# Performance work log

Hardware: AMD Instinct MI355X
Metric: run time of the kernel (lower is better)

## Reference

```python
import jax, jax.numpy as jnp
import numpy as np

N = 100000   # nodes
E = 1600000  # edges (before self-loops)
F_IN = 128
H = 64
G = 512      # graphs in batch


def _add_self_loops(edge_index, n):
    loop = jnp.arange(n, dtype=edge_index.dtype)
    src = jnp.concatenate([edge_index[0], loop])
    dst = jnp.concatenate([edge_index[1], loop])
    return src, dst


def _gcn_norm(src, dst, n):
    # PyG GCNConv: deg over targets with self-loops, norm = d^-1/2[src]*d^-1/2[dst]
    deg = jax.ops.segment_sum(jnp.ones_like(dst, dtype=jnp.float32), dst, num_segments=n)
    dinv = jnp.where(deg > 0, jax.lax.rsqrt(deg), 0.0)
    return dinv[src] * dinv[dst]


def _gcn_conv(x, src, dst, norm, W, b):
    xw = x @ W                                # [N, H]
    msg = xw[src] * norm[:, None]             # [E+N, H] gather + scale
    out = jax.ops.segment_sum(msg, dst, num_segments=x.shape[0])
    return out + b


def setup_inputs() -> dict:
    key = jax.random.key(0)
    ks = jax.random.split(key, 9)
    x = jax.random.normal(ks[0], (N, F_IN), dtype=jnp.float32)
    edge_index = jax.random.randint(ks[1], (2, E), 0, N, dtype=jnp.int32)
    batch = jnp.sort(jax.random.randint(ks[2], (N,), 0, G, dtype=jnp.int32))
    s1 = 1.0 / np.sqrt(F_IN)
    s2 = 1.0 / np.sqrt(H)
    W1 = jax.random.uniform(ks[3], (F_IN, H), jnp.float32, -s1, s1)
    b1 = jnp.zeros((H,), jnp.float32)
    W2 = jax.random.uniform(ks[4], (H, H), jnp.float32, -s2, s2)
    b2 = jnp.zeros((H,), jnp.float32)
    Wl = jax.random.uniform(ks[5], (H, 1), jnp.float32, -s2, s2)
    bl = jnp.zeros((1,), jnp.float32)
    return {"x": x, "edge_index": edge_index, "batch": batch,
            "W1": W1, "b1": b1, "W2": W2, "b2": b2, "Wl": Wl, "bl": bl}


def reference(x, edge_index, batch, W1, b1, W2, b2, Wl, bl):
    n = x.shape[0]
    src, dst = _add_self_loops(edge_index, n)
    norm = _gcn_norm(src, dst, n)
    h = jax.nn.relu(_gcn_conv(x, src, dst, norm, W1, b1))
    h = jax.nn.relu(_gcn_conv(h, src, dst, norm, W2, b2))
    # global mean pool over graphs
    sums = jax.ops.segment_sum(h, batch, num_segments=G)          # [G, H]
    cnt = jax.ops.segment_sum(jnp.ones((n,), jnp.float32), batch, num_segments=G)
    pooled = sums / jnp.maximum(cnt, 1.0)[:, None]
    return jax.nn.sigmoid(pooled @ Wl + bl)                        # [G, 1]
```

## Files before the change

### kernel.cpp

```cpp
#include <hip/hip_runtime.h>
#include <hip/hip_bf16.h>
#include <cmath>

#define F_IN 128
#define HDIM 64
#define NPB 128
#define NB1 512
#define CAP 2560

typedef __attribute__((ext_vector_type(8))) short bf16x8;
typedef __attribute__((ext_vector_type(4))) float f32x4;
typedef __attribute__((ext_vector_type(2))) float f32x2;

__device__ __forceinline__ unsigned short f2bf(float f) {
    __hip_bfloat16 h = __float2bfloat16(f);
    union { __hip_bfloat16 h; unsigned short u; } c; c.h = h; return c.u;
}
__device__ __forceinline__ unsigned char f2fp8(float f) {
    int p = __builtin_amdgcn_cvt_pk_fp8_f32(f, f, 0, false);
    return (unsigned char)(p & 0xff);
}
__device__ __forceinline__ void fp8x8_acc(uint2 v, float* a) {
    f32x2 f;
    f = __builtin_amdgcn_cvt_pk_f32_fp8(v.x, false); a[0] += f.x; a[1] += f.y;
    f = __builtin_amdgcn_cvt_pk_f32_fp8(v.x, true);  a[2] += f.x; a[3] += f.y;
    f = __builtin_amdgcn_cvt_pk_f32_fp8(v.y, false); a[4] += f.x; a[5] += f.y;
    f = __builtin_amdgcn_cvt_pk_f32_fp8(v.y, true);  a[6] += f.x; a[7] += f.y;
}

__device__ __forceinline__ void gather_rows(const int* __restrict__ col,
                                            const uint2* __restrict__ xws,
                                            int L, int s, int end, float* a) {
    int e = s;
    int c[8];
    bool have = (e + 8 <= end);
    if (have) {
#pragma unroll
        for (int i = 0; i < 8; ++i) c[i] = col[e + i];
    }
    while (have) {
        uint2 v0 = xws[(size_t)c[0] * 8 + L];
        uint2 v1 = xws[(size_t)c[1] * 8 + L];
        uint2 v2 = xws[(size_t)c[2] * 8 + L];
        uint2 v3 = xws[(size_t)c[3] * 8 + L];
        uint2 v4 = xws[(size_t)c[4] * 8 + L];
        uint2 v5 = xws[(size_t)c[5] * 8 + L];
        uint2 v6 = xws[(size_t)c[6] * 8 + L];
        uint2 v7 = xws[(size_t)c[7] * 8 + L];
        int e2 = e + 8;
        bool nxt = (e2 + 8 <= end);
        int d[8];
#pragma unroll
        for (int i = 0; i < 8; ++i) d[i] = nxt ? col[e2 + i] : 0;
        fp8x8_acc(v0, a); fp8x8_acc(v1, a); fp8x8_acc(v2, a); fp8x8_acc(v3, a);
        fp8x8_acc(v4, a); fp8x8_acc(v5, a); fp8x8_acc(v6, a); fp8x8_acc(v7, a);
#pragma unroll
        for (int i = 0; i < 8; ++i) c[i] = d[i];
        e = e2; have = nxt;
    }
    for (; e < end; ++e)
        fp8x8_acc(xws[(size_t)col[e] * 8 + L], a);
}


__launch_bounds__(256)
__global__ void k_init(const float* __restrict__ W1, const float* __restrict__ W2,
                       unsigned short* __restrict__ w1t, unsigned short* __restrict__ w2t,
                       const int* __restrict__ batch, int* __restrict__ gstart,
                       int n, int G, int* __restrict__ gcnt, int nbuk,
                       float* __restrict__ pooled) {
    int t = blockIdx.x * 256 + threadIdx.x;
    if (t < F_IN * 64) {
        int c = t & 63, k = t >> 6;
        w1t[c * F_IN + k] = f2bf(W1[t]);
        return;
    }
    t -= F_IN * 64;
    if (t < HDIM * 64) {
        int c = t & 63, k = t >> 6;
        w2t[c * HDIM + k] = f2bf(W2[t]);
        return;
    }
    t -= HDIM * 64;
    if (t <= G) {
        int g = t;
        int lo = 0, hi = n;
        while (lo < hi) {
            int mid = (lo + hi) >> 1;
            if (batch[mid] < g) lo = mid + 1; else hi = mid;
        }
        gstart[g] = lo;
        return;
    }
    t -= G + 1;
    if (t < nbuk) { gcnt[t] = 0; return; }
    t -= nbuk;
    if (t < G * HDIM) pooled[t] = 0.0f;
}


__launch_bounds__(256)
__global__ void p_place(const int* __restrict__ src, const int* __restrict__ dst,
                        int* __restrict__ gcnt, int* __restrict__ pairs,
                        int E, int nbuk, int chunk) {
    __shared__ int hist[1024];
    __shared__ int cur[1024];
    int tid = threadIdx.x;
    for (int i = tid; i < nbuk; i += 256) hist[i] = 0;
    __syncthreads();
    int lo = blockIdx.x * chunk, hi = min(E, lo + chunk);
    for (int e = lo + tid; e < hi; e += 256)
        atomicAdd(&hist[dst[e] >> 7], 1);
    __syncthreads();
    for (int i = tid; i < nbuk; i += 256) {
        int c = hist[i];
        cur[i] = i * CAP + (c ? atomicAdd(&gcnt[i], c) : 0);
    }
    __syncthreads();
    for (int e = lo + tid; e < hi; e += 256) {
        int d = dst[e];
        int pos = atomicAdd(&cur[d >> 7], 1);
        pairs[pos] = (src[e] << 7) | (d & 127);
    }
}


__launch_bounds__(256)
__global__ void p2_csr(const int* __restrict__ pairs, const int* __restrict__ bucket_cnt,
                       float* __restrict__ dinv, int* __restrict__ col,
                       int4* __restrict__ slot_hdr, int n) {
    __shared__ int plds[CAP];
    __shared__ int dl[128];
    __shared__ int sc[128];
    __shared__ int cur[128];
    __shared__ int h64[64];
    __shared__ int s64[64];
    int b = blockIdx.x, tid = threadIdx.x;
    int nlo = b << 7;
    int eb = b * CAP;
    int cnt = bucket_cnt[b];
    if (tid < 128) dl[tid] = 0;
    if (tid < 64) h64[tid] = 0;
    __syncthreads();
    for (int i = tid; i < cnt; i += 256) {
        int v = pairs[eb + i];
        plds[i] = v;
        atomicAdd(&dl[v & 127], 1);
    }
    __syncthreads();
    int d0 = 0, excl = 0;
    if (tid < 128) { d0 = dl[tid]; sc[tid] = d0; }
    __syncthreads();
    for (int off = 1; off < 128; off <<= 1) {
        int a = (tid >= off && tid < 128) ? sc[tid - off] : 0;
        __syncthreads();
        if (tid < 128) sc[tid] += a;
        __syncthreads();
    }
    if (tid < 128) {
        excl = sc[tid] - d0;
        int node = nlo + tid;
        float dv = rsqrtf((float)(d0 + 1));
        if (node < n) dinv[node] = dv;
        cur[tid] = eb + excl;
        atomicAdd(&h64[min(d0, 63)], 1);
    }
    __syncthreads();
    if (tid == 0) { int run = 0; for (int i = 0; i < 64; ++i) { s64[i] = run; run += h64[i]; } }
    __syncthreads();
    if (tid < 64) h64[tid] = 0;
    __syncthreads();
    if (tid < 128) {
        int node = nlo + tid;
        int bin = min(d0, 63);
        int pos = s64[bin] + atomicAdd(&h64[bin], 1);
        int4 hdr;
        hdr.x = (node < n) ? node : 0x7fffffff;
        hdr.y = eb + excl;
        hdr.z = d0;
        hdr.w = __float_as_int(rsqrtf((float)(d0 + 1)));
        slot_hdr[nlo + pos] = hdr;
    }
    __syncthreads();
    for (int i = tid; i < cnt; i += 256) {
        unsigned int v = (unsigned int)plds[i];
        int pos = atomicAdd(&cur[v & 127], 1);
        col[pos] = (int)(v >> 7);
    }
}


template <int K>
__launch_bounds__(256)
__global__ void matmul_mfma(const float* __restrict__ X, const unsigned short* __restrict__ Wt,
                            const float* __restrict__ dinv, unsigned char* __restrict__ out,
                            int n) {
    constexpr int KS  = K / 32;
    constexpr int LDX = K + 8;
    __shared__ unsigned short Xs[64 * LDX];
    __shared__ unsigned short Ws[64 * LDX];
    int tid = threadIdx.x;
    int rowbase = blockIdx.x * 64;
    for (int i = tid; i < 64 * (K / 8); i += 256) {
        int r = i / (K / 8), ch = i % (K / 8);
        *(bf16x8*)(Ws + r * LDX + ch * 8) = ((const bf16x8*)Wt)[i];
    }
    {
        const float4* X4 = (const float4*)X;
        for (int i = tid; i < 64 * (K / 4); i += 256) {
            int r = i / (K / 4), k4 = i % (K / 4);
            ushort4 u = { 0, 0, 0, 0 };
            int gr = rowbase + r;
            if (gr < n) {
                float4 v = X4[(size_t)gr * (K / 4) + k4];
                u.x = f2bf(v.x); u.y = f2bf(v.y); u.z = f2bf(v.z); u.w = f2bf(v.w);
            }
            *(ushort4*)(Xs + r * LDX + k4 * 4) = u;
        }
    }
    __syncthreads();
    int wave = tid >> 6, lane = tid & 63;
    int q = lane >> 4, nn = lane & 15;
    f32x4 acc[4] = {{0,0,0,0},{0,0,0,0},{0,0,0,0},{0,0,0,0}};
    int mrow = wave * 16 + nn;
#pragma unroll
    for (int s = 0; s < KS; ++s) {
        bf16x8 af = *(const bf16x8*)(Xs + mrow * LDX + s * 32 + q * 8);
#pragma unroll
        for (int c = 0; c < 4; ++c) {
            bf16x8 bf = *(const bf16x8*)(Ws + (c * 16 + nn) * LDX + s * 32 + q * 8);
            acc[c] = __builtin_amdgcn_mfma_f32_16x16x32_bf16(af, bf, acc[c], 0, 0, 0);
        }
    }
#pragma unroll
    for (int r = 0; r < 4; ++r) {
        int row = rowbase + wave * 16 + q * 4 + r;
        if (row >= n) continue;
        float dv = dinv[row];
#pragma unroll
        for (int c = 0; c < 4; ++c)
            out[(size_t)row * HDIM + c * 16 + nn] = f2fp8(acc[c][r] * dv);
    }
}


__launch_bounds__(256)
__global__ void gather1_mm2(const int4* __restrict__ slot_hdr, const int* __restrict__ col,
                            const uint2* __restrict__ xws, const float* __restrict__ bias,
                            const unsigned short* __restrict__ w2t,
                            unsigned char* __restrict__ out8, int nslots, int n) {
    __shared__ unsigned short Hs[32 * 72];
    __shared__ unsigned short Ws[64 * 72];
    __shared__ int   snode[32];
    __shared__ float sdinv[32];

    int tid = threadIdx.x;
    int ls = tid >> 3;
    int L  = tid & 7;
    int slot = blockIdx.x * 32 + ls;

    for (int i = tid; i < 64 * 8; i += 256) {
        int r = i >> 3, ch = i & 7;
        *(bf16x8*)(Ws + r * 72 + ch * 8) = ((const bf16x8*)w2t)[i];
    }

    int node = 0x7fffffff;
    float dv = 0.0f;
    float a[8] = {0, 0, 0, 0, 0, 0, 0, 0};
    if (slot < nslots) {
        int4 hdr = slot_hdr[slot];
        node = hdr.x;
        if (node < n) {
            int s = hdr.y, end = s + hdr.z;
            dv = __int_as_float(hdr.w);
            fp8x8_acc(xws[(size_t)node * 8 + L], a);
            gather_rows(col, xws, L, s, end, a);
        }
    }
    if (L == 0) { snode[ls] = node; sdinv[ls] = dv; }
    {
        int f0 = L * 8;
        bf16x8 o;
        if (node < n) {
#pragma unroll
            for (int j = 0; j < 8; ++j)
                o[j] = (short)f2bf(fmaxf(fmaf(a[j], dv, bias[f0 + j]), 0.0f));
        } else {
            short z[8] = {0,0,0,0,0,0,0,0};
            o = *(bf16x8*)z;
        }
        *(bf16x8*)(Hs + ls * 72 + L * 8) = o;
    }
    __syncthreads();

    int wave = tid >> 6, lane = tid & 63;
    int q = lane >> 4, nn = lane & 15;
    int mt  = wave & 1;
    int nt0 = (wave >> 1) * 2;
    f32x4 acc[2] = {{0,0,0,0},{0,0,0,0}};
#pragma unroll
    for (int s = 0; s < 2; ++s) {
        bf16x8 af = *(const bf16x8*)(Hs + (mt * 16 + nn) * 72 + s * 32 + q * 8);
#pragma unroll
        for (int t = 0; t < 2; ++t) {
            bf16x8 bf = *(const bf16x8*)(Ws + ((nt0 + t) * 16 + nn) * 72 + s * 32 + q * 8);
            acc[t] = __builtin_amdgcn_mfma_f32_16x16x32_bf16(af, bf, acc[t], 0, 0, 0);
        }
    }
#pragma unroll
    for (int r = 0; r < 4; ++r) {
        int lslot = mt * 16 + q * 4 + r;
        int nd = snode[lslot];
        if (nd >= n) continue;
        float dvr = sdinv[lslot];
#pragma unroll
        for (int t = 0; t < 2; ++t)
            out8[(size_t)nd * HDIM + (nt0 + t) * 16 + nn] = f2fp8(acc[t][r] * dvr);
    }
}


__launch_bounds__(256)
__global__ void gather2_pool(const int4* __restrict__ slot_hdr, const int* __restrict__ col,
                             const uint2* __restrict__ xws, const float* __restrict__ bias,
                             const int* __restrict__ batch, float* __restrict__ pooled,
                             int nslots, int n, int G) {
    __shared__ float lpool[4][HDIM];
    __shared__ int sg[32];
    __shared__ int sgmin;
    int tid = threadIdx.x;
    int ls = tid >> 3;
    int L  = tid & 7;
    int slot = blockIdx.x * 32 + ls;

    lpool[tid >> 6][tid & 63] = 0.0f;
    if (tid == 0) sgmin = 0x7fffffff;

    int node = 0x7fffffff;
    float dv = 0.0f;
    int s = 0, deg = 0;
    if (slot < nslots) {
        int4 hdr = slot_hdr[slot];
        node = hdr.x;
        if (node < n) { s = hdr.y; deg = hdr.z; dv = __int_as_float(hdr.w); }
    }
    if (L == 0) {
        int g = (node < n) ? batch[node] : 0x7fffffff;
        sg[ls] = g;
        if (node < n) atomicMin(&sgmin, g);
    }

    float a[8] = {0, 0, 0, 0, 0, 0, 0, 0};
    if (node < n) {
        fp8x8_acc(xws[(size_t)node * 8 + L], a);
        gather_rows(col, xws, L, s, s + deg, a);
    }
    __syncthreads();

    int gmin = sgmin;
    if (node < n) {
        int g  = sg[ls];
        int gl = g - gmin;
        int f0 = L * 8;
        if (gl < 4) {
#pragma unroll
            for (int j = 0; j < 8; ++j)
                atomicAdd(&lpool[gl][f0 + j], fmaxf(fmaf(a[j], dv, bias[f0 + j]), 0.0f));
        } else {
#pragma unroll
            for (int j = 0; j < 8; ++j)
                atomicAdd(&pooled[(size_t)g * HDIM + f0 + j],
                          fmaxf(fmaf(a[j], dv, bias[f0 + j]), 0.0f));
        }
    }
    __syncthreads();

    if (gmin != 0x7fffffff) {
        int r = tid >> 6, f = tid & 63;
        float v = lpool[r][f];
        int gg = gmin + r;
        if (v != 0.0f && gg < G)
            atomicAdd(&pooled[(size_t)gg * HDIM + f], v);
    }
}


__launch_bounds__(256)
__global__ void head(const float* __restrict__ pooled, const int* __restrict__ gstart,
                     const float* __restrict__ Wl, const float* __restrict__ bl,
                     float* __restrict__ out, int G) {
    int g = blockIdx.x * 4 + (threadIdx.x >> 6);
    int f = threadIdx.x & 63;
    if (g >= G) return;
    float cnt = fmaxf((float)(gstart[g + 1] - gstart[g]), 1.0f);
    float v = pooled[(size_t)g * HDIM + f] * Wl[f] * (1.0f / cnt);
#pragma unroll
    for (int off = 32; off; off >>= 1) v += __shfl_down(v, off, 64);
    if (f == 0) out[g] = 1.0f / (1.0f + expf(-(v + bl[0])));
}


extern "C" void kernel_launch(void* const* d_in, const int* in_sizes, int n_in,
                              void* d_out, int out_size, void* d_ws, size_t ws_size,
                              hipStream_t stream) {
    const float* x   = (const float*)d_in[0];
    const int* ei    = (const int*)d_in[1];
    const int* batch = (const int*)d_in[2];
    const float* W1  = (const float*)d_in[3];
    const float* b1  = (const float*)d_in[4];
    const float* W2  = (const float*)d_in[5];
    const float* b2  = (const float*)d_in[6];
    const float* Wl  = (const float*)d_in[7];
    const float* bl  = (const float*)d_in[8];
    float* out = (float*)d_out;

    const int n = in_sizes[0] / F_IN;
    const int E = in_sizes[1] / 2;
    const int G = out_size;

    const int* srcp = ei;
    const int* dstp = ei + E;

    int nbuk = (n + NPB - 1) / NPB;
    int nslots = nbuk * NPB;

    char* wsb = (char*)d_ws;
    auto alloc = [&](size_t bytes) { char* p = wsb; wsb += (bytes + 255) & ~(size_t)255; return p; };
    float* dinv       = (float*)alloc((size_t)n * 4);
    int4*  slot_hdr   = (int4*)alloc((size_t)nslots * 16);
    int*   gcnt       = (int*)alloc(1024 * 4);
    int*   pairs      = (int*)alloc((size_t)nbuk * CAP * 4);
    int*   colx       = (int*)alloc((size_t)nbuk * CAP * 4);
    unsigned short* w1t  = (unsigned short*)alloc((size_t)F_IN * HDIM * 2);
    unsigned short* w2t  = (unsigned short*)alloc((size_t)HDIM * HDIM * 2);
    unsigned char*  xws8 = (unsigned char*)alloc((size_t)n * HDIM);
    unsigned char*  xws8b= (unsigned char*)alloc((size_t)n * HDIM);
    float* pooled     = (float*)alloc((size_t)G * HDIM * 4);
    int*   gstart     = (int*)alloc(((size_t)G + 1) * 4);

    const int TB = 256;
    int gMM  = (n + 63) / 64;
    int chunk = (E + NB1 - 1) / NB1;
    int gS   = (nslots + 31) / 32;
    int initWork = F_IN * 64 + HDIM * 64 + (G + 1) + nbuk + G * HDIM;
    int gInit = (initWork + TB - 1) / TB;

    k_init<<<gInit, TB, 0, stream>>>(W1, W2, w1t, w2t, batch, gstart, n, G,
                                     gcnt, nbuk, pooled);
    p_place<<<NB1, TB, 0, stream>>>(srcp, dstp, gcnt, pairs, E, nbuk, chunk);
    p2_csr<<<nbuk, TB, 0, stream>>>(pairs, gcnt, dinv, colx, slot_hdr, n);
    matmul_mfma<F_IN><<<gMM, TB, 0, stream>>>(x, w1t, dinv, xws8, n);
    gather1_mm2<<<gS, TB, 0, stream>>>(slot_hdr, colx, (const uint2*)xws8,
                                       b1, w2t, xws8b, nslots, n);
    gather2_pool<<<gS, TB, 0, stream>>>(slot_hdr, colx, (const uint2*)xws8b,
                                        b2, batch, pooled, nslots, n, G);
    head<<<(G + 3) / 4, TB, 0, stream>>>(pooled, gstart, Wl, bl, out, G);
}
```

Baseline: 262.2 us.

## Gather fp8 rows with 4 lanes of 16 bytes and 64 nodes per block

The two gather kernels now give each node 4 lanes that each load 16 bytes (uint4), instead of 8 lanes loading 8 bytes, so each block covers 64 nodes rather than 32. The edge loop drops its software-prefetched column indices for a plain 8-wide unrolled loop and handles the tail with a clamped, masked 8-wide batch. gather1_mm2 then runs a 64x64 MFMA tile, with each wave computing all four column tiles. The aim is fewer, wider memory requests and more nodes in flight per block, at the cost of more registers per thread and less parallelism within each row.

```diff
diff --git a/kernel.cpp b/kernel.cpp
--- a/kernel.cpp
+++ b/kernel.cpp
@@ -20,46 +20,48 @@
     int p = __builtin_amdgcn_cvt_pk_fp8_f32(f, f, 0, false);
     return (unsigned char)(p & 0xff);
 }
-__device__ __forceinline__ void fp8x8_acc(uint2 v, float* a) {
+__device__ __forceinline__ void fp8x16_acc(uint4 v, float* a) {
     f32x2 f;
-    f = __builtin_amdgcn_cvt_pk_f32_fp8(v.x, false); a[0] += f.x; a[1] += f.y;
-    f = __builtin_amdgcn_cvt_pk_f32_fp8(v.x, true);  a[2] += f.x; a[3] += f.y;
-    f = __builtin_amdgcn_cvt_pk_f32_fp8(v.y, false); a[4] += f.x; a[5] += f.y;
-    f = __builtin_amdgcn_cvt_pk_f32_fp8(v.y, true);  a[6] += f.x; a[7] += f.y;
-}
-
-__device__ __forceinline__ void gather_rows(const int* __restrict__ col,
-                                            const uint2* __restrict__ xws,
-                                            int L, int s, int end, float* a) {
+    f = __builtin_amdgcn_cvt_pk_f32_fp8(v.x, false); a[0]  += f.x; a[1]  += f.y;
+    f = __builtin_amdgcn_cvt_pk_f32_fp8(v.x, true);  a[2]  += f.x; a[3]  += f.y;
+    f = __builtin_amdgcn_cvt_pk_f32_fp8(v.y, false); a[4]  += f.x; a[5]  += f.y;
+    f = __builtin_amdgcn_cvt_pk_f32_fp8(v.y, true);  a[6]  += f.x; a[7]  += f.y;
+    f = __builtin_amdgcn_cvt_pk_f32_fp8(v.z, false); a[8]  += f.x; a[9]  += f.y;
+    f = __builtin_amdgcn_cvt_pk_f32_fp8(v.z, true);  a[10] += f.x; a[11] += f.y;
+    f = __builtin_amdgcn_cvt_pk_f32_fp8(v.w, false); a[12] += f.x; a[13] += f.y;
+    f = __builtin_amdgcn_cvt_pk_f32_fp8(v.w, true);  a[14] += f.x; a[15] += f.y;
+}
+
+__device__ __forceinline__ void gather_rows4(const int* __restrict__ col,
+                                             const uint4* __restrict__ xq,
+                                             int L, int s, int end, float* a) {
     int e = s;
-    int c[8];
-    bool have = (e + 8 <= end);
-    if (have) {
-#pragma unroll
-        for (int i = 0; i < 8; ++i) c[i] = col[e + i];
-    }
-    while (have) {
-        uint2 v0 = xws[(size_t)c[0] * 8 + L];
-        uint2 v1 = xws[(size_t)c[1] * 8 + L];
-        uint2 v2 = xws[(size_t)c[2] * 8 + L];
-        uint2 v3 = xws[(size_t)c[3] * 8 + L];
-        uint2 v4 = xws[(size_t)c[4] * 8 + L];
-        uint2 v5 = xws[(size_t)c[5] * 8 + L];
-        uint2 v6 = xws[(size_t)c[6] * 8 + L];
-        uint2 v7 = xws[(size_t)c[7] * 8 + L];
-        int e2 = e + 8;
-        bool nxt = (e2 + 8 <= end);
-        int d[8];
-#pragma unroll
-        for (int i = 0; i < 8; ++i) d[i] = nxt ? col[e2 + i] : 0;
-        fp8x8_acc(v0, a); fp8x8_acc(v1, a); fp8x8_acc(v2, a); fp8x8_acc(v3, a);
-        fp8x8_acc(v4, a); fp8x8_acc(v5, a); fp8x8_acc(v6, a); fp8x8_acc(v7, a);
-#pragma unroll
-        for (int i = 0; i < 8; ++i) c[i] = d[i];
-        e = e2; have = nxt;
-    }
-    for (; e < end; ++e)
-        fp8x8_acc(xws[(size_t)col[e] * 8 + L], a);
+    for (; e + 8 <= end; e += 8) {
+        int c0 = col[e + 0], c1 = col[e + 1], c2 = col[e + 2], c3 = col[e + 3];
+        int c4 = col[e + 4], c5 = col[e + 5], c6 = col[e + 6], c7 = col[e + 7];
+        uint4 v0 = xq[(size_t)c0 * 4 + L];
+        uint4 v1 = xq[(size_t)c1 * 4 + L];
+        uint4 v2 = xq[(size_t)c2 * 4 + L];
+        uint4 v3 = xq[(size_t)c3 * 4 + L];
+        uint4 v4 = xq[(size_t)c4 * 4 + L];
+        uint4 v5 = xq[(size_t)c5 * 4 + L];
+        uint4 v6 = xq[(size_t)c6 * 4 + L];
+        uint4 v7 = xq[(size_t)c7 * 4 + L];
+        fp8x16_acc(v0, a); fp8x16_acc(v1, a); fp8x16_acc(v2, a); fp8x16_acc(v3, a);
+        fp8x16_acc(v4, a); fp8x16_acc(v5, a); fp8x16_acc(v6, a); fp8x16_acc(v7, a);
+    }
+    if (e < end) {
+        int last = end - 1;
+        int c[8];
+#pragma unroll
+        for (int i = 0; i < 8; ++i) c[i] = col[min(e + i, last)];
+        uint4 v[8];
+#pragma unroll
+        for (int i = 0; i < 8; ++i) v[i] = xq[(size_t)c[i] * 4 + L];
+#pragma unroll
+        for (int i = 0; i < 8; ++i)
+            if (e + i < end) fp8x16_acc(v[i], a);
+    }
 }
 
 
@@ -246,18 +248,18 @@
 
 __launch_bounds__(256)
 __global__ void gather1_mm2(const int4* __restrict__ slot_hdr, const int* __restrict__ col,
-                            const uint2* __restrict__ xws, const float* __restrict__ bias,
+                            const uint4* __restrict__ xq, const float* __restrict__ bias,
                             const unsigned short* __restrict__ w2t,
                             unsigned char* __restrict__ out8, int nslots, int n) {
-    __shared__ unsigned short Hs[32 * 72];
+    __shared__ unsigned short Hs[64 * 72];
     __shared__ unsigned short Ws[64 * 72];
-    __shared__ int   snode[32];
-    __shared__ float sdinv[32];
+    __shared__ int   snode[64];
+    __shared__ float sdinv[64];
 
     int tid = threadIdx.x;
-    int ls = tid >> 3;
-    int L  = tid & 7;
-    int slot = blockIdx.x * 32 + ls;
+    int ls = tid >> 2;
+    int L  = tid & 3;
+    int slot = blockIdx.x * 64 + ls;
 
     for (int i = tid; i < 64 * 8; i += 256) {
         int r = i >> 3, ch = i & 7;
@@ -266,72 +268,72 @@
 
     int node = 0x7fffffff;
     float dv = 0.0f;
-    float a[8] = {0, 0, 0, 0, 0, 0, 0, 0};
+    float a[16] = {0,0,0,0,0,0,0,0,0,0,0,0,0,0,0,0};
     if (slot < nslots) {
         int4 hdr = slot_hdr[slot];
         node = hdr.x;
         if (node < n) {
-            int s = hdr.y, end = s + hdr.z;
             dv = __int_as_float(hdr.w);
-            fp8x8_acc(xws[(size_t)node * 8 + L], a);
-            gather_rows(col, xws, L, s, end, a);
+            fp8x16_acc(xq[(size_t)node * 4 + L], a);
+            gather_rows4(col, xq, L, hdr.y, hdr.y + hdr.z, a);
         }
     }
     if (L == 0) { snode[ls] = node; sdinv[ls] = dv; }
     {
-        int f0 = L * 8;
-        bf16x8 o;
+        int f0 = L * 16;
+        bf16x8 o0, o1;
         if (node < n) {
 #pragma unroll
-            for (int j = 0; j < 8; ++j)
-                o[j] = (short)f2bf(fmaxf(fmaf(a[j], dv, bias[f0 + j]), 0.0f));
+            for (int j = 0; j < 8; ++j) {
+                o0[j] = (short)f2bf(fmaxf(fmaf(a[j],     dv, bias[f0 + j]),     0.0f));
+                o1[j] = (short)f2bf(fmaxf(fmaf(a[8 + j], dv, bias[f0 + 8 + j]), 0.0f));
+            }
         } else {
             short z[8] = {0,0,0,0,0,0,0,0};
-            o = *(bf16x8*)z;
-        }
-        *(bf16x8*)(Hs + ls * 72 + L * 8) = o;
+            o0 = *(bf16x8*)z; o1 = o0;
+        }
+        *(bf16x8*)(Hs + ls * 72 + f0)     = o0;
+        *(bf16x8*)(Hs + ls * 72 + f0 + 8) = o1;
     }
     __syncthreads();
 
     int wave = tid >> 6, lane = tid & 63;
     int q = lane >> 4, nn = lane & 15;
-    int mt  = wave & 1;
-    int nt0 = (wave >> 1) * 2;
-    f32x4 acc[2] = {{0,0,0,0},{0,0,0,0}};
+    f32x4 acc[4] = {{0,0,0,0},{0,0,0,0},{0,0,0,0},{0,0,0,0}};
 #pragma unroll
     for (int s = 0; s < 2; ++s) {
-        bf16x8 af = *(const bf16x8*)(Hs + (mt * 16 + nn) * 72 + s * 32 + q * 8);
-#pragma unroll
-        for (int t = 0; t < 2; ++t) {
-            bf16x8 bf = *(const bf16x8*)(Ws + ((nt0 + t) * 16 + nn) * 72 + s * 32 + q * 8);
+        bf16x8 af = *(const bf16x8*)(Hs + (wave * 16 + nn) * 72 + s * 32 + q * 8);
+#pragma unroll
+        for (int t = 0; t < 4; ++t) {
+            bf16x8 bf = *(const bf16x8*)(Ws + (t * 16 + nn) * 72 + s * 32 + q * 8);
             acc[t] = __builtin_amdgcn_mfma_f32_16x16x32_bf16(af, bf, acc[t], 0, 0, 0);
         }
     }
 #pragma unroll
     for (int r = 0; r < 4; ++r) {
-        int lslot = mt * 16 + q * 4 + r;
+        int lslot = wave * 16 + q * 4 + r;
         int nd = snode[lslot];
         if (nd >= n) continue;
         float dvr = sdinv[lslot];
 #pragma unroll
-        for (int t = 0; t < 2; ++t)
-            out8[(size_t)nd * HDIM + (nt0 + t) * 16 + nn] = f2fp8(acc[t][r] * dvr);
+        for (int t = 0; t < 4; ++t)
+            out8[(size_t)nd * HDIM + t * 16 + nn] = f2fp8(acc[t][r] * dvr);
     }
 }
 
 
 __launch_bounds__(256)
 __global__ void gather2_pool(const int4* __restrict__ slot_hdr, const int* __restrict__ col,
-                             const uint2* __restrict__ xws, const float* __restrict__ bias,
+                             const uint4* __restrict__ xq, const float* __restrict__ bias,
                              const int* __restrict__ batch, float* __restrict__ pooled,
                              int nslots, int n, int G) {
     __shared__ float lpool[4][HDIM];
-    __shared__ int sg[32];
+    __shared__ int sg[64];
     __shared__ int sgmin;
     int tid = threadIdx.x;
-    int ls = tid >> 3;
-    int L  = tid & 7;
-    int slot = blockIdx.x * 32 + ls;
+    int ls = tid >> 2;
+    int L  = tid & 3;
+    int slot = blockIdx.x * 64 + ls;
 
     lpool[tid >> 6][tid & 63] = 0.0f;
     if (tid == 0) sgmin = 0x7fffffff;
@@ -350,10 +352,10 @@
         if (node < n) atomicMin(&sgmin, g);
     }
 
-    float a[8] = {0, 0, 0, 0, 0, 0, 0, 0};
+    float a[16] = {0,0,0,0,0,0,0,0,0,0,0,0,0,0,0,0};
     if (node < n) {
-        fp8x8_acc(xws[(size_t)node * 8 + L], a);
-        gather_rows(col, xws, L, s, s + deg, a);
+        fp8x16_acc(xq[(size_t)node * 4 + L], a);
+        gather_rows4(col, xq, L, s, s + deg, a);
     }
     __syncthreads();
 
@@ -361,14 +363,14 @@
     if (node < n) {
         int g  = sg[ls];
         int gl = g - gmin;
-        int f0 = L * 8;
+        int f0 = L * 16;
         if (gl < 4) {
 #pragma unroll
-            for (int j = 0; j < 8; ++j)
+            for (int j = 0; j < 16; ++j)
                 atomicAdd(&lpool[gl][f0 + j], fmaxf(fmaf(a[j], dv, bias[f0 + j]), 0.0f));
         } else {
 #pragma unroll
-            for (int j = 0; j < 8; ++j)
+            for (int j = 0; j < 16; ++j)
                 atomicAdd(&pooled[(size_t)g * HDIM + f0 + j],
                           fmaxf(fmaf(a[j], dv, bias[f0 + j]), 0.0f));
         }
@@ -441,7 +443,7 @@
     const int TB = 256;
     int gMM  = (n + 63) / 64;
     int chunk = (E + NB1 - 1) / NB1;
-    int gS   = (nslots + 31) / 32;
+    int gS   = (nslots + 63) / 64;
     int initWork = F_IN * 64 + HDIM * 64 + (G + 1) + nbuk + G * HDIM;
     int gInit = (initWork + TB - 1) / TB;
 
@@ -450,9 +452,9 @@
     p_place<<<NB1, TB, 0, stream>>>(srcp, dstp, gcnt, pairs, E, nbuk, chunk);
     p2_csr<<<nbuk, TB, 0, stream>>>(pairs, gcnt, dinv, colx, slot_hdr, n);
     matmul_mfma<F_IN><<<gMM, TB, 0, stream>>>(x, w1t, dinv, xws8, n);
-    gather1_mm2<<<gS, TB, 0, stream>>>(slot_hdr, colx, (const uint2*)xws8,
+    gather1_mm2<<<gS, TB, 0, stream>>>(slot_hdr, colx, (const uint4*)xws8,
                                        b1, w2t, xws8b, nslots, n);
-    gather2_pool<<<gS, TB, 0, stream>>>(slot_hdr, colx, (const uint2*)xws8b,
+    gather2_pool<<<gS, TB, 0, stream>>>(slot_hdr, colx, (const uint4*)xws8b,
                                         b2, batch, pooled, nslots, n, G);
     head<<<(G + 3) / 4, TB, 0, stream>>>(pooled, gstart, Wl, bl, out, G);
 }
```

After: 259.8 us. Within noise of the previous version (-0.9%).

## Use persistent grid-stride gather kernels with degree-phase group remapping

Applied to the files above, without the earlier changes.

Both gather kernels become persistent: a fixed grid of at most 2048 blocks loops over 32-node slot groups, so W2 is staged into shared memory once per block instead of once per group. Group indices are remapped so that each stride-phase visits the quarter-buckets in reverse order, which changes the load-balancing order across blocks, presumably spreading heavy-degree groups. The software-pipelined column-index prefetch in gather_rows is replaced by a simpler loop that loads col inline. The cost is extra __syncthreads per iteration and the loss of explicit index prefetch, which may expose latency.

```diff
diff --git a/kernel.cpp b/kernel.cpp
--- a/kernel.cpp
+++ b/kernel.cpp
@@ -7,6 +7,7 @@
 #define NPB 128
 #define NB1 512
 #define CAP 2560
+#define GGRID 2048
 
 typedef __attribute__((ext_vector_type(8))) short bf16x8;
 typedef __attribute__((ext_vector_type(4))) float f32x4;
@@ -32,34 +33,26 @@
                                             const uint2* __restrict__ xws,
                                             int L, int s, int end, float* a) {
     int e = s;
-    int c[8];
-    bool have = (e + 8 <= end);
-    if (have) {
-#pragma unroll
-        for (int i = 0; i < 8; ++i) c[i] = col[e + i];
-    }
-    while (have) {
-        uint2 v0 = xws[(size_t)c[0] * 8 + L];
-        uint2 v1 = xws[(size_t)c[1] * 8 + L];
-        uint2 v2 = xws[(size_t)c[2] * 8 + L];
-        uint2 v3 = xws[(size_t)c[3] * 8 + L];
-        uint2 v4 = xws[(size_t)c[4] * 8 + L];
-        uint2 v5 = xws[(size_t)c[5] * 8 + L];
-        uint2 v6 = xws[(size_t)c[6] * 8 + L];
-        uint2 v7 = xws[(size_t)c[7] * 8 + L];
-        int e2 = e + 8;
-        bool nxt = (e2 + 8 <= end);
-        int d[8];
-#pragma unroll
-        for (int i = 0; i < 8; ++i) d[i] = nxt ? col[e2 + i] : 0;
+    for (; e + 8 <= end; e += 8) {
+        uint2 v0 = xws[(size_t)col[e + 0] * 8 + L];
+        uint2 v1 = xws[(size_t)col[e + 1] * 8 + L];
+        uint2 v2 = xws[(size_t)col[e + 2] * 8 + L];
+        uint2 v3 = xws[(size_t)col[e + 3] * 8 + L];
+        uint2 v4 = xws[(size_t)col[e + 4] * 8 + L];
+        uint2 v5 = xws[(size_t)col[e + 5] * 8 + L];
+        uint2 v6 = xws[(size_t)col[e + 6] * 8 + L];
+        uint2 v7 = xws[(size_t)col[e + 7] * 8 + L];
         fp8x8_acc(v0, a); fp8x8_acc(v1, a); fp8x8_acc(v2, a); fp8x8_acc(v3, a);
         fp8x8_acc(v4, a); fp8x8_acc(v5, a); fp8x8_acc(v6, a); fp8x8_acc(v7, a);
-#pragma unroll
-        for (int i = 0; i < 8; ++i) c[i] = d[i];
-        e = e2; have = nxt;
     }
     for (; e < end; ++e)
         fp8x8_acc(xws[(size_t)col[e] * 8 + L], a);
+}
+
+__device__ __forceinline__ int remap_group(int v, int nbuk) {
+    int phase = v / nbuk;
+    int b = v - phase * nbuk;
+    return b * 4 + (3 - phase);
 }
 
 
@@ -248,7 +241,7 @@
 __global__ void gather1_mm2(const int4* __restrict__ slot_hdr, const int* __restrict__ col,
                             const uint2* __restrict__ xws, const float* __restrict__ bias,
                             const unsigned short* __restrict__ w2t,
-                            unsigned char* __restrict__ out8, int nslots, int n) {
+                            unsigned char* __restrict__ out8, int ngroups, int nbuk, int n) {
     __shared__ unsigned short Hs[32 * 72];
     __shared__ unsigned short Ws[64 * 72];
     __shared__ int   snode[32];
@@ -257,65 +250,69 @@
     int tid = threadIdx.x;
     int ls = tid >> 3;
     int L  = tid & 7;
-    int slot = blockIdx.x * 32 + ls;
 
     for (int i = tid; i < 64 * 8; i += 256) {
         int r = i >> 3, ch = i & 7;
         *(bf16x8*)(Ws + r * 72 + ch * 8) = ((const bf16x8*)w2t)[i];
     }
 
-    int node = 0x7fffffff;
-    float dv = 0.0f;
-    float a[8] = {0, 0, 0, 0, 0, 0, 0, 0};
-    if (slot < nslots) {
-        int4 hdr = slot_hdr[slot];
-        node = hdr.x;
-        if (node < n) {
-            int s = hdr.y, end = s + hdr.z;
-            dv = __int_as_float(hdr.w);
-            fp8x8_acc(xws[(size_t)node * 8 + L], a);
-            gather_rows(col, xws, L, s, end, a);
-        }
-    }
-    if (L == 0) { snode[ls] = node; sdinv[ls] = dv; }
-    {
-        int f0 = L * 8;
-        bf16x8 o;
-        if (node < n) {
-#pragma unroll
-            for (int j = 0; j < 8; ++j)
-                o[j] = (short)f2bf(fmaxf(fmaf(a[j], dv, bias[f0 + j]), 0.0f));
-        } else {
-            short z[8] = {0,0,0,0,0,0,0,0};
-            o = *(bf16x8*)z;
-        }
-        *(bf16x8*)(Hs + ls * 72 + L * 8) = o;
-    }
-    __syncthreads();
-
-    int wave = tid >> 6, lane = tid & 63;
-    int q = lane >> 4, nn = lane & 15;
-    int mt  = wave & 1;
-    int nt0 = (wave >> 1) * 2;
-    f32x4 acc[2] = {{0,0,0,0},{0,0,0,0}};
-#pragma unroll
-    for (int s = 0; s < 2; ++s) {
-        bf16x8 af = *(const bf16x8*)(Hs + (mt * 16 + nn) * 72 + s * 32 + q * 8);
-#pragma unroll
-        for (int t = 0; t < 2; ++t) {
-            bf16x8 bf = *(const bf16x8*)(Ws + ((nt0 + t) * 16 + nn) * 72 + s * 32 + q * 8);
-            acc[t] = __builtin_amdgcn_mfma_f32_16x16x32_bf16(af, bf, acc[t], 0, 0, 0);
-        }
-    }
-#pragma unroll
-    for (int r = 0; r < 4; ++r) {
-        int lslot = mt * 16 + q * 4 + r;
-        int nd = snode[lslot];
-        if (nd >= n) continue;
-        float dvr = sdinv[lslot];
-#pragma unroll
-        for (int t = 0; t < 2; ++t)
-            out8[(size_t)nd * HDIM + (nt0 + t) * 16 + nn] = f2fp8(acc[t][r] * dvr);
+    for (int v = blockIdx.x; v < ngroups; v += gridDim.x) {
+        int grp = remap_group(v, nbuk);
+        int slot = grp * 32 + ls;
+
+        int node = 0x7fffffff;
+        float dv = 0.0f;
+        float a[8] = {0, 0, 0, 0, 0, 0, 0, 0};
+        {
+            int4 hdr = slot_hdr[slot];
+            node = hdr.x;
+            if (node < n) {
+                dv = __int_as_float(hdr.w);
+                fp8x8_acc(xws[(size_t)node * 8 + L], a);
+                gather_rows(col, xws, L, hdr.y, hdr.y + hdr.z, a);
+            }
+        }
+        if (L == 0) { snode[ls] = node; sdinv[ls] = dv; }
+        {
+            int f0 = L * 8;
+            bf16x8 o;
+            if (node < n) {
+#pragma unroll
+                for (int j = 0; j < 8; ++j)
+                    o[j] = (short)f2bf(fmaxf(fmaf(a[j], dv, bias[f0 + j]), 0.0f));
+            } else {
+                short z[8] = {0,0,0,0,0,0,0,0};
+                o = *(bf16x8*)z;
+            }
+            *(bf16x8*)(Hs + ls * 72 + L * 8) = o;
+        }
+        __syncthreads();
+
+        int wave = tid >> 6, lane = tid & 63;
+        int q = lane >> 4, nn = lane & 15;
+        int mt  = wave & 1;
+        int nt0 = (wave >> 1) * 2;
+        f32x4 acc[2] = {{0,0,0,0},{0,0,0,0}};
+#pragma unroll
+        for (int s = 0; s < 2; ++s) {
+            bf16x8 af = *(const bf16x8*)(Hs + (mt * 16 + nn) * 72 + s * 32 + q * 8);
+#pragma unroll
+            for (int t = 0; t < 2; ++t) {
+                bf16x8 bf = *(const bf16x8*)(Ws + ((nt0 + t) * 16 + nn) * 72 + s * 32 + q * 8);
+                acc[t] = __builtin_amdgcn_mfma_f32_16x16x32_bf16(af, bf, acc[t], 0, 0, 0);
+            }
+        }
+#pragma unroll
+        for (int r = 0; r < 4; ++r) {
+            int lslot = mt * 16 + q * 4 + r;
+            int nd = snode[lslot];
+            if (nd >= n) continue;
+            float dvr = sdinv[lslot];
+#pragma unroll
+            for (int t = 0; t < 2; ++t)
+                out8[(size_t)nd * HDIM + (nt0 + t) * 16 + nn] = f2fp8(acc[t][r] * dvr);
+        }
+        __syncthreads();
     }
 }
 
@@ -324,63 +321,69 @@
 __global__ void gather2_pool(const int4* __restrict__ slot_hdr, const int* __restrict__ col,
                              const uint2* __restrict__ xws, const float* __restrict__ bias,
                              const int* __restrict__ batch, float* __restrict__ pooled,
-                             int nslots, int n, int G) {
+                             int ngroups, int nbuk, int n, int G) {
     __shared__ float lpool[4][HDIM];
     __shared__ int sg[32];
     __shared__ int sgmin;
     int tid = threadIdx.x;
     int ls = tid >> 3;
     int L  = tid & 7;
-    int slot = blockIdx.x * 32 + ls;
-
-    lpool[tid >> 6][tid & 63] = 0.0f;
-    if (tid == 0) sgmin = 0x7fffffff;
-
-    int node = 0x7fffffff;
-    float dv = 0.0f;
-    int s = 0, deg = 0;
-    if (slot < nslots) {
-        int4 hdr = slot_hdr[slot];
-        node = hdr.x;
-        if (node < n) { s = hdr.y; deg = hdr.z; dv = __int_as_float(hdr.w); }
-    }
-    if (L == 0) {
-        int g = (node < n) ? batch[node] : 0x7fffffff;
-        sg[ls] = g;
-        if (node < n) atomicMin(&sgmin, g);
-    }
-
-    float a[8] = {0, 0, 0, 0, 0, 0, 0, 0};
-    if (node < n) {
-        fp8x8_acc(xws[(size_t)node * 8 + L], a);
-        gather_rows(col, xws, L, s, s + deg, a);
-    }
-    __syncthreads();
-
-    int gmin = sgmin;
-    if (node < n) {
-        int g  = sg[ls];
-        int gl = g - gmin;
-        int f0 = L * 8;
-        if (gl < 4) {
-#pragma unroll
-            for (int j = 0; j < 8; ++j)
-                atomicAdd(&lpool[gl][f0 + j], fmaxf(fmaf(a[j], dv, bias[f0 + j]), 0.0f));
-        } else {
-#pragma unroll
-            for (int j = 0; j < 8; ++j)
-                atomicAdd(&pooled[(size_t)g * HDIM + f0 + j],
-                          fmaxf(fmaf(a[j], dv, bias[f0 + j]), 0.0f));
-        }
-    }
-    __syncthreads();
-
-    if (gmin != 0x7fffffff) {
-        int r = tid >> 6, f = tid & 63;
-        float v = lpool[r][f];
-        int gg = gmin + r;
-        if (v != 0.0f && gg < G)
-            atomicAdd(&pooled[(size_t)gg * HDIM + f], v);
+
+    for (int v = blockIdx.x; v < ngroups; v += gridDim.x) {
+        int grp = remap_group(v, nbuk);
+        int slot = grp * 32 + ls;
+
+        lpool[tid >> 6][tid & 63] = 0.0f;
+        if (tid == 0) sgmin = 0x7fffffff;
+        __syncthreads();
+
+        int node = 0x7fffffff;
+        float dv = 0.0f;
+        int s = 0, deg = 0;
+        {
+            int4 hdr = slot_hdr[slot];
+            node = hdr.x;
+            if (node < n) { s = hdr.y; deg = hdr.z; dv = __int_as_float(hdr.w); }
+        }
+        if (L == 0) {
+            int g = (node < n) ? batch[node] : 0x7fffffff;
+            sg[ls] = g;
+            if (node < n) atomicMin(&sgmin, g);
+        }
+
+        float a[8] = {0, 0, 0, 0, 0, 0, 0, 0};
+        if (node < n) {
+            fp8x8_acc(xws[(size_t)node * 8 + L], a);
+            gather_rows(col, xws, L, s, s + deg, a);
+        }
+        __syncthreads();
+
+        int gmin = sgmin;
+        if (node < n) {
+            int g  = sg[ls];
+            int gl = g - gmin;
+            int f0 = L * 8;
+            if (gl < 4) {
+#pragma unroll
+                for (int j = 0; j < 8; ++j)
+                    atomicAdd(&lpool[gl][f0 + j], fmaxf(fmaf(a[j], dv, bias[f0 + j]), 0.0f));
+            } else {
+#pragma unroll
+                for (int j = 0; j < 8; ++j)
+                    atomicAdd(&pooled[(size_t)g * HDIM + f0 + j],
+                              fmaxf(fmaf(a[j], dv, bias[f0 + j]), 0.0f));
+            }
+        }
+        __syncthreads();
+
+        if (gmin != 0x7fffffff) {
+            int r = tid >> 6, f = tid & 63;
+            float vv = lpool[r][f];
+            int gg = gmin + r;
+            if (vv != 0.0f && gg < G)
+                atomicAdd(&pooled[(size_t)gg * HDIM + f], vv);
+        }
+        __syncthreads();
     }
 }
 
@@ -423,6 +426,7 @@
 
     int nbuk = (n + NPB - 1) / NPB;
     int nslots = nbuk * NPB;
+    int ngroups = nbuk * 4;
 
     char* wsb = (char*)d_ws;
     auto alloc = [&](size_t bytes) { char* p = wsb; wsb += (bytes + 255) & ~(size_t)255; return p; };
@@ -441,7 +445,7 @@
     const int TB = 256;
     int gMM  = (n + 63) / 64;
     int chunk = (E + NB1 - 1) / NB1;
-    int gS   = (nslots + 31) / 32;
+    int gGat = min(GGRID, ngroups);
     int initWork = F_IN * 64 + HDIM * 64 + (G + 1) + nbuk + G * HDIM;
     int gInit = (initWork + TB - 1) / TB;
 
@@ -450,9 +454,9 @@
     p_place<<<NB1, TB, 0, stream>>>(srcp, dstp, gcnt, pairs, E, nbuk, chunk);
     p2_csr<<<nbuk, TB, 0, stream>>>(pairs, gcnt, dinv, colx, slot_hdr, n);
     matmul_mfma<F_IN><<<gMM, TB, 0, stream>>>(x, w1t, dinv, xws8, n);
-    gather1_mm2<<<gS, TB, 0, stream>>>(slot_hdr, colx, (const uint2*)xws8,
-                                       b1, w2t, xws8b, nslots, n);
-    gather2_pool<<<gS, TB, 0, stream>>>(slot_hdr, colx, (const uint2*)xws8b,
-                                        b2, batch, pooled, nslots, n, G);
+    gather1_mm2<<<gGat, TB, 0, stream>>>(slot_hdr, colx, (const uint2*)xws8,
+                                         b1, w2t, xws8b, ngroups, nbuk, n);
+    gather2_pool<<<gGat, TB, 0, stream>>>(slot_hdr, colx, (const uint2*)xws8b,
+                                          b2, batch, pooled, ngroups, nbuk, n, G);
     head<<<(G + 3) / 4, TB, 0, stream>>>(pooled, gstart, Wl, bl, out, G);
 }
```

New measurement: 251.6 us. 1.04x faster.
